# Performance work log

Hardware: AMD Instinct MI355X
Metric: run time of the kernel (lower is better)

Reference implementation:

```python
import jax, jax.numpy as jnp
import numpy as np

D_MODEL = 1024
N_HEADS = 16
D_FF = 4 * D_MODEL
EPS = 1e-5


def _layer_norm(x, g, b):
    mu = jnp.mean(x, axis=-1, keepdims=True)
    var = jnp.mean(jnp.square(x - mu), axis=-1, keepdims=True)
    return (x - mu) * jax.lax.rsqrt(var + EPS) * g + b


def _mha(x, Wq, Wk, Wv, Wo, causal):
    B, S, D = x.shape
    H = N_HEADS
    Dh = D // H
    q = (x @ Wq).reshape(B, S, H, Dh)
    k = (x @ Wk).reshape(B, S, H, Dh)
    v = (x @ Wv).reshape(B, S, H, Dh)
    scores = jnp.einsum('bqhd,bkhd->bhqk', q, k) / jnp.sqrt(jnp.asarray(Dh, x.dtype))
    if causal:
        mask = jnp.tril(jnp.ones((S, S), dtype=bool))  # [S,S] causal mask
        scores = jnp.where(mask, scores, jnp.asarray(-1e9, x.dtype))
    attn = jax.nn.softmax(scores, axis=-1)
    out = jnp.einsum('bhqk,bkhd->bqhd', attn, v).reshape(B, S, D)
    return out @ Wo


def _ffn(x, W1, b1, W2, b2):
    return jax.nn.relu(x @ W1 + b1) @ W2 + b2


def setup_inputs() -> dict:
    key = jax.random.key(0)
    ks = jax.random.split(key, 12)
    sd = 1.0 / np.sqrt(D_MODEL)
    sf = 1.0 / np.sqrt(D_FF)
    B, S = 4, 1024
    return {
        'X': jax.random.normal(ks[0], (B, S, D_MODEL), jnp.float32),
        'Wq1': jax.random.normal(ks[1], (D_MODEL, D_MODEL), jnp.float32) * sd,
        'Wk1': jax.random.normal(ks[2], (D_MODEL, D_MODEL), jnp.float32) * sd,
        'Wv1': jax.random.normal(ks[3], (D_MODEL, D_MODEL), jnp.float32) * sd,
        'Wo1': jax.random.normal(ks[4], (D_MODEL, D_MODEL), jnp.float32) * sd,
        'Wq2': jax.random.normal(ks[5], (D_MODEL, D_MODEL), jnp.float32) * sd,
        'Wk2': jax.random.normal(ks[6], (D_MODEL, D_MODEL), jnp.float32) * sd,
        'Wv2': jax.random.normal(ks[7], (D_MODEL, D_MODEL), jnp.float32) * sd,
        'Wo2': jax.random.normal(ks[8], (D_MODEL, D_MODEL), jnp.float32) * sd,
        'ln_g': jnp.ones((D_MODEL,), jnp.float32),
        'ln_b': jnp.zeros((D_MODEL,), jnp.float32),
        'W1': jax.random.normal(ks[9], (D_MODEL, D_FF), jnp.float32) * sd,
        'b1': jnp.zeros((D_FF,), jnp.float32),
        'W2': jax.random.normal(ks[10], (D_FF, D_MODEL), jnp.float32) * sf,
        'b2': jnp.zeros((D_MODEL,), jnp.float32),
    }


def reference(X, Wq1, Wk1, Wv1, Wo1, Wq2, Wk2, Wv2, Wo2, ln_g, ln_b, W1, b1, W2, b2):
    # Faithful to the torch module (including its unusual residual wiring
    # and the single shared LayerNorm used at all three sites).
    masked = _mha(X, Wq1, Wk1, Wv1, Wo1, causal=True)
    norm_masked = X + _layer_norm(masked, ln_g, ln_b)
    attn2 = _mha(norm_masked, Wq2, Wk2, Wv2, Wo2, causal=False)
    norm_attn2 = attn2 + _layer_norm(attn2, ln_g, ln_b)
    ff = _ffn(norm_attn2, W1, b1, W2, b2)
    return norm_attn2 + _layer_norm(ff, ln_g, ln_b)
```

## Files before the change

### kernel.cpp

```cpp
#include <hip/hip_runtime.h>
#include <hip/hip_bf16.h>

#define D_MODEL 1024
#define N_HEADS 16
#define DH 64
#define D_FF   4096
#define SEQ    1024
#define BATCH  4
#define TOK    (BATCH*SEQ)
#define EPS    1e-5f
#define SCALE  0.125f
#define QSCL   0.18033688f

typedef unsigned short USHORT;
typedef __attribute__((ext_vector_type(8))) short short8v;
typedef __attribute__((ext_vector_type(4))) float f32x4;

__device__ __forceinline__ USHORT f2bf(float f) {
    unsigned int u; __builtin_memcpy(&u, &f, 4);
    u += 0x7fffu + ((u >> 16) & 1u);
    return (USHORT)(u >> 16);
}
__device__ __forceinline__ float bf2f(USHORT s) {
    unsigned int u = ((unsigned int)s) << 16;
    float f; __builtin_memcpy(&f, &u, 4);
    return f;
}

__device__ __forceinline__ short8v ld_frag(const USHORT* lds, int row, int c8) {
    return *reinterpret_cast<const short8v*>(
        &lds[row * 64 + (((c8) ^ (row & 7)) << 3)]);
}
__device__ __forceinline__ short8v ld128(const USHORT* lds, int row, int cu) {
    return *reinterpret_cast<const short8v*>(
        &lds[row * 128 + (((cu) ^ (row & 15)) << 3)]);
}

#define GLDS(gsrc, ldst) \
    __builtin_amdgcn_global_load_lds( \
        (const __attribute__((address_space(1))) void*)(gsrc), \
        (__attribute__((address_space(3))) void*)(ldst), 16, 0, 0)

#define WAITVM(n) asm volatile("s_waitcnt vmcnt(" #n ")" ::: "memory")

__global__ __launch_bounds__(512) void gemm_k256_kernel(
    const USHORT* __restrict__ A, const USHORT* __restrict__ Bt,
    float* __restrict__ Cf, USHORT* __restrict__ Cb, USHORT* __restrict__ Ck,
    USHORT* __restrict__ VtOut,
    int M, int N, int K, const float* __restrict__ bias, int relu, int qkv)
{
    __shared__ USHORT As[2][256 * 64];
    __shared__ USHORT Bs[2][256 * 64];

    const int tid = threadIdx.x;
    const int l   = tid & 63;
    const int w   = tid >> 6;
    const int wr  = w >> 2, wc = w & 3;
    const int lr  = l & 15, lg = l >> 4;

    const int gx  = gridDim.x;
    const int nwg = gx * gridDim.y;
    const int lin = blockIdx.y * gx + blockIdx.x;
    const int swz = (lin & 7) * (nwg >> 3) + (lin >> 3);
    const int m0  = (swz / gx) * 256, n0 = (swz % gx) * 256;

    const USHORT* aS[4]; const USHORT* bS[4]; int dOf[4];
#pragma unroll
    for (int p = 0; p < 4; ++p) {
        const int q = p * 512 + tid;
        const int row = q >> 3, cu = q & 7;
        const int cs = ((cu ^ (row & 7)) << 3);
        aS[p] = A  + (size_t)(m0 + row) * K + cs;
        bS[p] = Bt + (size_t)(n0 + row) * K + cs;
        dOf[p] = (p * 512 + w * 64) * 8;
    }

    auto stage = [&](int buf, int k0) {
#pragma unroll
        for (int p = 0; p < 4; ++p) {
            GLDS(aS[p] + k0, &As[buf][dOf[p]]);
            GLDS(bS[p] + k0, &Bs[buf][dOf[p]]);
        }
    };

    f32x4 acc[8][4];
#pragma unroll
    for (int i = 0; i < 8; ++i)
#pragma unroll
        for (int j = 0; j < 4; ++j) acc[i][j] = (f32x4){0.f, 0.f, 0.f, 0.f};

    const int nk = K >> 6;
    stage(0, 0);

    for (int t = 0; t < nk; ++t) {
        const int cur = t & 1;
        if (t + 1 < nk) {
            stage(cur ^ 1, (t + 1) << 6);
            WAITVM(8);
        } else {
            WAITVM(0);
        }
        __builtin_amdgcn_s_barrier();

#pragma unroll
        for (int ks = 0; ks < 2; ++ks) {
            short8v bfr[4];
#pragma unroll
            for (int ni = 0; ni < 4; ++ni)
                bfr[ni] = ld_frag(Bs[cur], wc * 64 + ni * 16 + lr, ks * 4 + lg);
            __builtin_amdgcn_s_setprio(1);
#pragma unroll
            for (int mi = 0; mi < 8; ++mi) {
                short8v af = ld_frag(As[cur], wr * 128 + mi * 16 + lr, ks * 4 + lg);
#pragma unroll
                for (int ni = 0; ni < 4; ++ni)
                    acc[mi][ni] = __builtin_amdgcn_mfma_f32_16x16x32_bf16(
                        af, bfr[ni], acc[mi][ni], 0, 0, 0);
            }
            __builtin_amdgcn_s_setprio(0);
        }
        __builtin_amdgcn_s_barrier();
    }

    if (qkv) {
#pragma unroll
        for (int mi = 0; mi < 8; ++mi) {
            const int row = m0 + wr * 128 + mi * 16 + (l >> 4) * 4;
#pragma unroll
            for (int ni = 0; ni < 4; ++ni) {
                const int col = n0 + wc * 64 + ni * 16 + lr;
                if (col < 2048) {
                    USHORT* dst = (col < 1024) ? Cb : Ck;
                    const float scl = (col < 1024) ? QSCL : 1.f;
                    const int c = col & 1023;
#pragma unroll
                    for (int j = 0; j < 4; ++j)
                        dst[(size_t)(row + j) * D_MODEL + c] =
                            f2bf(acc[mi][ni][j] * scl);
                } else {
                    const int c = col - 2048;
                    const int bb = row >> 10, jr = row & 1023;
                    const int hh = c >> 6, dd = c & 63;
                    ushort4 pk = make_ushort4(
                        f2bf(acc[mi][ni][0]), f2bf(acc[mi][ni][1]),
                        f2bf(acc[mi][ni][2]), f2bf(acc[mi][ni][3]));
                    *reinterpret_cast<ushort4*>(
                        &VtOut[((size_t)(bb * 16 + hh) * 64 + dd) * 1024 + jr]) = pk;
                }
            }
        }
    } else {
#pragma unroll
        for (int mi = 0; mi < 8; ++mi) {
            const int row = m0 + wr * 128 + mi * 16 + (l >> 4) * 4;
#pragma unroll
            for (int ni = 0; ni < 4; ++ni) {
                const int col = n0 + wc * 64 + ni * 16 + lr;
                const float bv = bias ? bias[col] : 0.f;
#pragma unroll
                for (int j = 0; j < 4; ++j) {
                    float v = acc[mi][ni][j] + bv;
                    if (relu) v = fmaxf(v, 0.f);
                    const size_t idx = (size_t)(row + j) * N + col;
                    if (Cf) Cf[idx] = v;
                    if (Cb) Cb[idx] = f2bf(v);
                }
            }
        }
    }
}

__global__ __launch_bounds__(256) void gemm_k64b_kernel(
    const USHORT* __restrict__ A, const USHORT* __restrict__ Bt,
    float* __restrict__ Cf, USHORT* __restrict__ Cb,
    int M, int N, int K, const float* __restrict__ bias, int relu)
{
    __shared__ USHORT As[3][64 * 64];
    __shared__ USHORT Bs[3][128 * 64];

    const int tid = threadIdx.x;
    const int l   = tid & 63;
    const int w   = tid >> 6;
    const int wr  = w >> 1, wc = w & 1;
    const int lr  = l & 15, lg = l >> 4;

    const int gx  = gridDim.x;
    const int nwg = gx * gridDim.y;
    const int lin = blockIdx.y * gx + blockIdx.x;
    const int swz = (lin & 7) * (nwg >> 3) + (lin >> 3);
    const int m0  = (swz / gx) * 64, n0 = (swz % gx) * 128;

    const int ar0 = tid >> 3,         ac0 = ((tid & 7) ^ (ar0 & 7)) << 3;
    const int ar1 = (256 + tid) >> 3, ac1 = (((256 + tid) & 7) ^ (ar1 & 7)) << 3;
    const USHORT* aS0 = A + (size_t)(m0 + ar0) * K + ac0;
    const USHORT* aS1 = A + (size_t)(m0 + ar1) * K + ac1;
    const int adOf0 = (w * 64) * 8;
    const int adOf1 = (256 + w * 64) * 8;

    const USHORT* bS[4]; int bdOf[4];
#pragma unroll
    for (int p = 0; p < 4; ++p) {
        const int q = p * 256 + tid;
        const int row = q >> 3, cu = q & 7;
        bS[p] = Bt + (size_t)(n0 + row) * K + ((cu ^ (row & 7)) << 3);
        bdOf[p] = (p * 256 + w * 64) * 8;
    }

    auto stage = [&](int buf, int k0) {
        GLDS(aS0 + k0, &As[buf][adOf0]);
        GLDS(aS1 + k0, &As[buf][adOf1]);
#pragma unroll
        for (int p = 0; p < 4; ++p)
            GLDS(bS[p] + k0, &Bs[buf][bdOf[p]]);
    };

    f32x4 acc[2][4];
#pragma unroll
    for (int i = 0; i < 2; ++i)
#pragma unroll
        for (int j = 0; j < 4; ++j) acc[i][j] = (f32x4){0.f, 0.f, 0.f, 0.f};

    const int nk = K >> 6;
    stage(0, 0);
    if (nk > 1) stage(1, 64);

    for (int t = 0; t < nk; ++t) {
        const int cur = t % 3;
        if (t + 1 < nk) { WAITVM(6); } else { WAITVM(0); }
        __builtin_amdgcn_s_barrier();
        if (t + 2 < nk) stage((t + 2) % 3, (t + 2) << 6);

#pragma unroll
        for (int ks = 0; ks < 2; ++ks) {
            short8v af[2], bfr[4];
#pragma unroll
            for (int mi = 0; mi < 2; ++mi)
                af[mi] = ld_frag(As[cur], wr * 32 + mi * 16 + lr, ks * 4 + lg);
#pragma unroll
            for (int ni = 0; ni < 4; ++ni)
                bfr[ni] = ld_frag(Bs[cur], wc * 64 + ni * 16 + lr, ks * 4 + lg);
            __builtin_amdgcn_s_setprio(1);
#pragma unroll
            for (int mi = 0; mi < 2; ++mi)
#pragma unroll
                for (int ni = 0; ni < 4; ++ni)
                    acc[mi][ni] = __builtin_amdgcn_mfma_f32_16x16x32_bf16(
                        af[mi], bfr[ni], acc[mi][ni], 0, 0, 0);
            __builtin_amdgcn_s_setprio(0);
        }
    }

#pragma unroll
    for (int mi = 0; mi < 2; ++mi) {
        const int row = m0 + wr * 32 + mi * 16 + (l >> 4) * 4;
#pragma unroll
        for (int ni = 0; ni < 4; ++ni) {
            const int col = n0 + wc * 64 + ni * 16 + lr;
            const float bv = bias ? bias[col] : 0.f;
#pragma unroll
            for (int j = 0; j < 4; ++j) {
                float v = acc[mi][ni][j] + bv;
                if (relu) v = fmaxf(v, 0.f);
                const size_t idx = (size_t)(row + j) * N + col;
                if (Cf) Cf[idx] = v;
                if (Cb) Cb[idx] = f2bf(v);
            }
        }
    }
}

struct TcvtB4 {
    const float* s0; const float* s1; const float* s2; const float* s3;
    USHORT* d0; USHORT* d1; USHORT* d2; USHORT* d3;
};

__device__ __forceinline__ void tcvt_body(
    const float* __restrict__ W, USHORT* __restrict__ Wt, int K, int N)
{
    __shared__ USHORT L[64][65];
    const int tid = threadIdx.x;
    const int tx = tid & 15, ty = tid >> 4;
    const int n0 = blockIdx.x * 64, k0 = blockIdx.y * 64;
#pragma unroll
    for (int r = 0; r < 4; ++r) {
        int kr = ty + 16 * r;
        float4 v = *reinterpret_cast<const float4*>(
            &W[(size_t)(k0 + kr) * N + n0 + tx * 4]);
        L[tx * 4 + 0][kr] = f2bf(v.x);
        L[tx * 4 + 1][kr] = f2bf(v.y);
        L[tx * 4 + 2][kr] = f2bf(v.z);
        L[tx * 4 + 3][kr] = f2bf(v.w);
    }
    __syncthreads();
#pragma unroll
    for (int r = 0; r < 4; ++r) {
        int nr = ty + 16 * r;
        ushort4 o = make_ushort4(L[nr][tx * 4 + 0], L[nr][tx * 4 + 1],
                                 L[nr][tx * 4 + 2], L[nr][tx * 4 + 3]);
        *reinterpret_cast<ushort4*>(&Wt[(size_t)(n0 + nr) * K + k0 + tx * 4]) = o;
    }
}

__global__ __launch_bounds__(256) void tcvt_kernel(
    const float* __restrict__ W, USHORT* __restrict__ Wt, int K, int N)
{
    tcvt_body(W, Wt, K, N);
}

__global__ __launch_bounds__(256) void tcvt4_kernel(TcvtB4 p, int K, int N)
{
    const int z = blockIdx.z;
    const float* W = (z == 0) ? p.s0 : (z == 1) ? p.s1 : (z == 2) ? p.s2 : p.s3;
    USHORT*    Wt = (z == 0) ? p.d0 : (z == 1) ? p.d1 : (z == 2) ? p.d2 : p.d3;
    tcvt_body(W, Wt, K, N);
}

__global__ __launch_bounds__(256) void f2b_kernel(
    const float* __restrict__ in, USHORT* __restrict__ out, int n4)
{
    int i = blockIdx.x * 256 + threadIdx.x;
    if (i < n4) {
        float4 v = reinterpret_cast<const float4*>(in)[i];
        reinterpret_cast<ushort4*>(out)[i] =
            make_ushort4(f2bf(v.x), f2bf(v.y), f2bf(v.z), f2bf(v.w));
    }
}

__global__ __launch_bounds__(256) void attn_mfma_kernel(
    const USHORT* __restrict__ Q, const USHORT* __restrict__ K,
    const USHORT* __restrict__ Vt, USHORT* __restrict__ O, int causal)
{
    __shared__ USHORT smem[40960];

    const int tid = threadIdx.x;
    const int l  = tid & 63;
    const int w  = tid >> 6;
    const int lr = l & 15;
    const int lg = l >> 4;

    const int lin = blockIdx.y * 16 + blockIdx.x;
    const int swz = (lin & 7) * 128 + (lin >> 3);
    const int qt = swz & 15;
    const int bh = swz >> 4;
    const int h = bh & 15, b = bh >> 4;
    const int q0 = qt * 64;

    const USHORT* gq  = Q  + (size_t)(b * SEQ + q0) * D_MODEL + h * DH;
    const USHORT* gk0 = K  + (size_t)b * SEQ * D_MODEL + h * DH;
    const USHORT* gv0 = Vt + (size_t)bh * DH * SEQ;

    auto stageK = [&](int buf, int kt) {
        USHORT* dst = smem + buf * 8192;
        const size_t base = (size_t)kt * 128 * 1024;
#pragma unroll
        for (int p = 0; p < 4; ++p) {
            const int q = p * 256 + tid;
            const int row = q >> 3, cu = q & 7;
            GLDS(gk0 + base + (size_t)row * 1024 + ((cu ^ (row & 7)) << 3),
                 dst + (p * 256 + w * 64) * 8);
        }
    };
    auto stageV = [&](int buf, int kt) {
        USHORT* dst = smem + 16384 + buf * 8192;
        const int j0 = kt * 128;
#pragma unroll
        for (int p = 0; p < 4; ++p) {
            const int q = p * 256 + tid;
            const int row = q >> 4, cu = q & 15;
            GLDS(gv0 + (size_t)row * 1024 + j0 + ((cu ^ (row & 15)) << 3),
                 dst + (p * 256 + w * 64) * 8);
        }
    };

#pragma unroll
    for (int p = 0; p < 2; ++p) {
        const int q = p * 256 + tid;
        const int row = q >> 3, cu = q & 7;
        GLDS(gq + (size_t)row * 1024 + ((cu ^ (row & 7)) << 3),
             smem + 32768 + (p * 256 + w * 64) * 8);
    }
    stageK(0, 0);
    stageV(0, 0);

    f32x4 oacc[4];
    float m_[4], l_[4];
#pragma unroll
    for (int r = 0; r < 4; ++r) { m_[r] = -1e30f; l_[r] = 0.f; }
#pragma unroll
    for (int d = 0; d < 4; ++d) oacc[d] = (f32x4){0.f, 0.f, 0.f, 0.f};

    __syncthreads();
    short8v qa0 = ld_frag(smem + 32768, w * 16 + lr, lg);
    short8v qa1 = ld_frag(smem + 32768, w * 16 + lr, 4 + lg);
    __syncthreads();
    USHORT* PsW = smem + 32768 + w * 2048;

    const int ntile = causal ? (qt >> 1) + 1 : (SEQ / 128);
    for (int kt = 0; kt < ntile; ++kt) {
        const int cur = kt & 1;
        if (kt + 1 < ntile) {
            stageK(cur ^ 1, kt + 1);
            stageV(cur ^ 1, kt + 1);
        }
        const int j0 = kt * 128;
        const USHORT* KsC = smem + cur * 8192;
        const USHORT* VsC = smem + 16384 + cur * 8192;

        f32x4 sa[8];
        __builtin_amdgcn_s_setprio(1);
#pragma unroll
        for (int jb = 0; jb < 8; ++jb) {
            sa[jb] = (f32x4){0.f, 0.f, 0.f, 0.f};
            sa[jb] = __builtin_amdgcn_mfma_f32_16x16x32_bf16(
                qa0, ld_frag(KsC, jb * 16 + lr, lg), sa[jb], 0, 0, 0);
            sa[jb] = __builtin_amdgcn_mfma_f32_16x16x32_bf16(
                qa1, ld_frag(KsC, jb * 16 + lr, 4 + lg), sa[jb], 0, 0, 0);
        }
        __builtin_amdgcn_s_setprio(0);

        if (causal && kt == ntile - 1) {
#pragma unroll
            for (int jb = 0; jb < 8; ++jb)
#pragma unroll
                for (int r = 0; r < 4; ++r)
                    if ((j0 + jb * 16 + lr) > (q0 + w * 16 + lg * 4 + r))
                        sa[jb][r] = -1e30f;
        }

        float tmloc[4];
#pragma unroll
        for (int r = 0; r < 4; ++r)
            tmloc[r] = fmaxf(fmaxf(fmaxf(sa[0][r], sa[1][r]),
                                   fmaxf(sa[2][r], sa[3][r])),
                             fmaxf(fmaxf(sa[4][r], sa[5][r]),
                                   fmaxf(sa[6][r], sa[7][r])));

        const bool anyf = (tmloc[0] > m_[0] + 8.f) | (tmloc[1] > m_[1] + 8.f) |
                          (tmloc[2] > m_[2] + 8.f) | (tmloc[3] > m_[3] + 8.f);
        const unsigned long long bal = __ballot(anyf);
        if ((bal >> (lg * 16)) & 0xFFFFull) {
#pragma unroll
            for (int r = 0; r < 4; ++r) {
                float tm = tmloc[r];
                tm = fmaxf(tm, __shfl_xor(tm, 1));
                tm = fmaxf(tm, __shfl_xor(tm, 2));
                tm = fmaxf(tm, __shfl_xor(tm, 4));
                tm = fmaxf(tm, __shfl_xor(tm, 8));
                if (tm > m_[r] + 8.f) {
                    float sc = exp2f(m_[r] - tm);
                    l_[r] *= sc;
#pragma unroll
                    for (int d = 0; d < 4; ++d) oacc[d][r] *= sc;
                    m_[r] = tm;
                }
            }
        }

#pragma unroll
        for (int r = 0; r < 4; ++r) {
            float rs_ = 0.f;
#pragma unroll
            for (int jb = 0; jb < 8; ++jb) {
                float p = exp2f(sa[jb][r] - m_[r]);
                sa[jb][r] = p;
                rs_ += p;
            }
            l_[r] += rs_;
        }

#pragma unroll
        for (int jb = 0; jb < 8; ++jb) {
            const int cu = jb * 2 + (lr >> 3), cl = lr & 7;
#pragma unroll
            for (int r = 0; r < 4; ++r) {
                const int row = lg * 4 + r;
                PsW[row * 128 + ((cu ^ (row & 15)) << 3) + cl] = f2bf(sa[jb][r]);
            }
        }

        __builtin_amdgcn_s_setprio(1);
#pragma unroll
        for (int ks = 0; ks < 4; ++ks) {
            short8v pa = ld128(PsW, lr, ks * 4 + lg);
#pragma unroll
            for (int d = 0; d < 4; ++d)
                oacc[d] = __builtin_amdgcn_mfma_f32_16x16x32_bf16(
                    pa, ld128(VsC, d * 16 + lr, ks * 4 + lg), oacc[d], 0, 0, 0);
        }
        __builtin_amdgcn_s_setprio(0);
        __syncthreads();
    }

    USHORT* go = O + (size_t)(b * SEQ + q0 + w * 16) * D_MODEL + h * DH;
#pragma unroll
    for (int r = 0; r < 4; ++r) {
        float lv = l_[r];
        lv += __shfl_xor(lv, 1);
        lv += __shfl_xor(lv, 2);
        lv += __shfl_xor(lv, 4);
        lv += __shfl_xor(lv, 8);
        const float inv = 1.f / lv;
        const int qrow = lg * 4 + r;
#pragma unroll
        for (int d = 0; d < 4; ++d)
            go[(size_t)qrow * D_MODEL + d * 16 + lr] = f2bf(oacc[d][r] * inv);
    }
}

__global__ __launch_bounds__(256) void ln_res_kernel(
    const USHORT* __restrict__ xb, const float* __restrict__ resf,
    const USHORT* __restrict__ resb,
    const float* __restrict__ g, const float* __restrict__ bta,
    float* __restrict__ outf, USHORT* __restrict__ outb)
{
    __shared__ float red[256];
    __shared__ float s_mu, s_rstd;

    const int row = blockIdx.x;
    const int tid = threadIdx.x;
    ushort4 xv = reinterpret_cast<const ushort4*>(xb + (size_t)row * D_MODEL)[tid];
    float vx = bf2f(xv.x), vy = bf2f(xv.y), vz = bf2f(xv.z), vw = bf2f(xv.w);

    red[tid] = vx + vy + vz + vw;
    __syncthreads();
    for (int s = 128; s > 0; s >>= 1) {
        if (tid < s) red[tid] += red[tid + s];
        __syncthreads();
    }
    if (tid == 0) s_mu = red[0] * (1.f / D_MODEL);
    __syncthreads();
    const float mu = s_mu;

    float dx = vx - mu, dy = vy - mu, dz = vz - mu, dw = vw - mu;
    red[tid] = dx * dx + dy * dy + dz * dz + dw * dw;
    __syncthreads();
    for (int s = 128; s > 0; s >>= 1) {
        if (tid < s) red[tid] += red[tid + s];
        __syncthreads();
    }
    if (tid == 0) s_rstd = rsqrtf(red[0] * (1.f / D_MODEL) + EPS);
    __syncthreads();
    const float rstd = s_rstd;

    float4 rv;
    if (resf) {
        rv = reinterpret_cast<const float4*>(resf + (size_t)row * D_MODEL)[tid];
    } else {
        ushort4 rb = reinterpret_cast<const ushort4*>(
            resb + (size_t)row * D_MODEL)[tid];
        rv = make_float4(bf2f(rb.x), bf2f(rb.y), bf2f(rb.z), bf2f(rb.w));
    }
    float4 gv = reinterpret_cast<const float4*>(g)[tid];
    float4 bv = reinterpret_cast<const float4*>(bta)[tid];

    float4 o;
    o.x = rv.x + dx * rstd * gv.x + bv.x;
    o.y = rv.y + dy * rstd * gv.y + bv.y;
    o.z = rv.z + dz * rstd * gv.z + bv.z;
    o.w = rv.w + dw * rstd * gv.w + bv.w;
    reinterpret_cast<float4*>(outf + (size_t)row * D_MODEL)[tid] = o;
    if (outb)
        reinterpret_cast<ushort4*>(outb + (size_t)row * D_MODEL)[tid] =
            make_ushort4(f2bf(o.x), f2bf(o.y), f2bf(o.z), f2bf(o.w));
}

extern "C" void kernel_launch(void* const* d_in, const int* in_sizes, int n_in,
                              void* d_out, int out_size, void* d_ws, size_t ws_size,
                              hipStream_t stream)
{
    const float* X    = (const float*)d_in[0];
    const float* Wq1  = (const float*)d_in[1];
    const float* Wk1  = (const float*)d_in[2];
    const float* Wv1  = (const float*)d_in[3];
    const float* Wo1  = (const float*)d_in[4];
    const float* Wq2  = (const float*)d_in[5];
    const float* Wk2  = (const float*)d_in[6];
    const float* Wv2  = (const float*)d_in[7];
    const float* Wo2  = (const float*)d_in[8];
    const float* ln_g = (const float*)d_in[9];
    const float* ln_b = (const float*)d_in[10];
    const float* W1   = (const float*)d_in[11];
    const float* b1   = (const float*)d_in[12];
    const float* W2   = (const float*)d_in[13];
    const float* b2   = (const float*)d_in[14];

    const size_t MI = 1024 * 1024;
    USHORT* ws16 = (USHORT*)d_ws;
    USHORT* Wqkv1t = ws16;
    USHORT* Wo1t   = ws16 + 3 * MI;
    USHORT* Wqkv2t = ws16 + 4 * MI;
    USHORT* Wo2t   = ws16 + 7 * MI;
    USHORT* W2t    = ws16 + 8 * MI;
    USHORT* Xb     = ws16 + 12 * MI;
    USHORT* W1t    = Xb;
    USHORT* qb     = ws16 + 16 * MI;
    USHORT* kb     = ws16 + 20 * MI;
    USHORT* Vtb    = ws16 + 24 * MI;
    USHORT* t0b    = ws16 + 28 * MI;
    USHORT* hb     = qb;
    USHORT* t2b    = ws16 + 32 * MI;
    USHORT* t1b    = ws16 + 36 * MI;
    float*  t2     = (float*)(ws16 + 40 * MI);

    auto gemm256 = [&](const USHORT* A, const USHORT* Bt, float* Cf, USHORT* Cb,
                       int M, int N, int K, const float* bias, int relu) {
        gemm_k256_kernel<<<dim3(N / 256, M / 256), 512, 0, stream>>>(
            A, Bt, Cf, Cb, nullptr, nullptr, M, N, K, bias, relu, 0);
    };
    auto gemm_qkv = [&](const USHORT* A, const USHORT* Bt) {
        gemm_k256_kernel<<<dim3(3072 / 256, TOK / 256), 512, 0, stream>>>(
            A, Bt, nullptr, qb, kb, Vtb, TOK, 3072, D_MODEL, nullptr, 0, 1);
    };
    auto gemm64b = [&](const USHORT* A, const USHORT* Bt, float* Cf, USHORT* Cb,
                       int M, int N, int K, const float* bias, int relu) {
        gemm_k64b_kernel<<<dim3(N / 128, M / 64), 256, 0, stream>>>(
            A, Bt, Cf, Cb, M, N, K, bias, relu);
    };

    dim3 agrid(SEQ / 64, BATCH * N_HEADS);

    {
        TcvtB4 p1{Wq1, Wk1, Wv1, Wo1,
                  Wqkv1t, Wqkv1t + 1 * MI, Wqkv1t + 2 * MI, Wo1t};
        tcvt4_kernel<<<dim3(16, 16, 4), 256, 0, stream>>>(p1, D_MODEL, D_MODEL);
        TcvtB4 p2{Wq2, Wk2, Wv2, Wo2,
                  Wqkv2t, Wqkv2t + 1 * MI, Wqkv2t + 2 * MI, Wo2t};
        tcvt4_kernel<<<dim3(16, 16, 4), 256, 0, stream>>>(p2, D_MODEL, D_MODEL);
    }
    tcvt_kernel<<<dim3(D_MODEL / 64, D_FF / 64), 256, 0, stream>>>(
        W2, W2t, D_FF, D_MODEL);
    f2b_kernel<<<dim3(4096), 256, 0, stream>>>(X, Xb, TOK * D_MODEL / 4);

    gemm_qkv(Xb, Wqkv1t);
    attn_mfma_kernel<<<agrid, 256, 0, stream>>>(qb, kb, Vtb, t0b, 1);
    gemm64b(t0b, Wo1t, nullptr, t1b, TOK, D_MODEL, D_MODEL, nullptr, 0);
    ln_res_kernel<<<dim3(TOK), 256, 0, stream>>>(t1b, X, nullptr,
                                                 ln_g, ln_b, t2, t2b);
    tcvt_kernel<<<dim3(D_FF / 64, D_MODEL / 64), 256, 0, stream>>>(
        W1, W1t, D_MODEL, D_FF);

    gemm_qkv(t2b, Wqkv2t);
    attn_mfma_kernel<<<agrid, 256, 0, stream>>>(qb, kb, Vtb, t0b, 0);
    gemm64b(t0b, Wo2t, nullptr, t1b, TOK, D_MODEL, D_MODEL, nullptr, 0);
    ln_res_kernel<<<dim3(TOK), 256, 0, stream>>>(t1b, nullptr, t1b,
                                                 ln_g, ln_b, t2, t2b);

    gemm256(t2b, W1t, nullptr, hb, TOK, D_FF, D_MODEL, b1, 1);
    gemm64b(hb, W2t, nullptr, t1b, TOK, D_MODEL, D_FF, b2, 0);
    ln_res_kernel<<<dim3(TOK), 256, 0, stream>>>(t1b, t2, nullptr,
                                                 ln_g, ln_b, (float*)d_out, nullptr);
}
```

Measured before the change: 371.2 us.

## Split-K the narrow-N GEMMs in two and reduce partials in the LayerNorm kernel

The 64x128-tile GEMM used for the output projections and FFN down-projection is replaced by a split-K variant that launches twice as many workgroups, each covering half of K and writing bf16 partials to separate buffers. The LayerNorm/residual kernel now sums the two partials and adds the bias, so the reduction and bias are folded into an existing pass. The pipeline drops from triple to double buffering with an extra barrier per iteration. This adds partial-buffer write/read traffic and bf16 rounding of partials in exchange for better occupancy on the 4096x1024 outputs.

```diff
diff --git a/kernel.cpp b/kernel.cpp
--- a/kernel.cpp
+++ b/kernel.cpp
@@ -170,13 +170,13 @@
     }
 }
 
-__global__ __launch_bounds__(256) void gemm_k64b_kernel(
+__global__ __launch_bounds__(256) void gemm_k64c_kernel(
     const USHORT* __restrict__ A, const USHORT* __restrict__ Bt,
-    float* __restrict__ Cf, USHORT* __restrict__ Cb,
-    int M, int N, int K, const float* __restrict__ bias, int relu)
-{
-    __shared__ USHORT As[3][64 * 64];
-    __shared__ USHORT Bs[3][128 * 64];
+    USHORT* __restrict__ Pa, USHORT* __restrict__ Pb,
+    int M, int N, int K)
+{
+    __shared__ USHORT As[2][64 * 64];
+    __shared__ USHORT Bs[2][128 * 64];
 
     const int tid = threadIdx.x;
     const int l   = tid & 63;
@@ -188,7 +188,13 @@
     const int nwg = gx * gridDim.y;
     const int lin = blockIdx.y * gx + blockIdx.x;
     const int swz = (lin & 7) * (nwg >> 3) + (lin >> 3);
-    const int m0  = (swz / gx) * 64, n0 = (swz % gx) * 128;
+    const int my  = swz / gx;
+    const int mt  = M >> 6;
+    const int part = my / mt;
+    const int m0  = (my % mt) * 64;
+    const int n0  = (swz % gx) * 128;
+    const int koff = part * (K >> 1);
+    USHORT* dst = part ? Pb : Pa;
 
     const int ar0 = tid >> 3,         ac0 = ((tid & 7) ^ (ar0 & 7)) << 3;
     const int ar1 = (256 + tid) >> 3, ac1 = (((256 + tid) & 7) ^ (ar1 & 7)) << 3;
@@ -220,15 +226,18 @@
 #pragma unroll
         for (int j = 0; j < 4; ++j) acc[i][j] = (f32x4){0.f, 0.f, 0.f, 0.f};
 
-    const int nk = K >> 6;
-    stage(0, 0);
-    if (nk > 1) stage(1, 64);
+    const int nk = K >> 7;
+    stage(0, koff);
 
     for (int t = 0; t < nk; ++t) {
-        const int cur = t % 3;
-        if (t + 1 < nk) { WAITVM(6); } else { WAITVM(0); }
+        const int cur = t & 1;
+        if (t + 1 < nk) {
+            stage(cur ^ 1, koff + ((t + 1) << 6));
+            WAITVM(6);
+        } else {
+            WAITVM(0);
+        }
         __builtin_amdgcn_s_barrier();
-        if (t + 2 < nk) stage((t + 2) % 3, (t + 2) << 6);
 
 #pragma unroll
         for (int ks = 0; ks < 2; ++ks) {
@@ -248,6 +257,7 @@
                         af[mi], bfr[ni], acc[mi][ni], 0, 0, 0);
             __builtin_amdgcn_s_setprio(0);
         }
+        __builtin_amdgcn_s_barrier();
     }
 
 #pragma unroll
@@ -256,15 +266,9 @@
 #pragma unroll
         for (int ni = 0; ni < 4; ++ni) {
             const int col = n0 + wc * 64 + ni * 16 + lr;
-            const float bv = bias ? bias[col] : 0.f;
-#pragma unroll
-            for (int j = 0; j < 4; ++j) {
-                float v = acc[mi][ni][j] + bv;
-                if (relu) v = fmaxf(v, 0.f);
-                const size_t idx = (size_t)(row + j) * N + col;
-                if (Cf) Cf[idx] = v;
-                if (Cb) Cb[idx] = f2bf(v);
-            }
+#pragma unroll
+            for (int j = 0; j < 4; ++j)
+                dst[(size_t)(row + j) * N + col] = f2bf(acc[mi][ni][j]);
         }
     }
 }
@@ -508,8 +512,9 @@
 }
 
 __global__ __launch_bounds__(256) void ln_res_kernel(
-    const USHORT* __restrict__ xb, const float* __restrict__ resf,
-    const USHORT* __restrict__ resb,
+    const USHORT* __restrict__ xb, const USHORT* __restrict__ xb2,
+    const float* __restrict__ biasx,
+    const float* __restrict__ resf, const USHORT* __restrict__ resb,
     const float* __restrict__ g, const float* __restrict__ bta,
     float* __restrict__ outf, USHORT* __restrict__ outb)
 {
@@ -520,6 +525,15 @@
     const int tid = threadIdx.x;
     ushort4 xv = reinterpret_cast<const ushort4*>(xb + (size_t)row * D_MODEL)[tid];
     float vx = bf2f(xv.x), vy = bf2f(xv.y), vz = bf2f(xv.z), vw = bf2f(xv.w);
+    if (xb2) {
+        ushort4 x2 = reinterpret_cast<const ushort4*>(
+            xb2 + (size_t)row * D_MODEL)[tid];
+        vx += bf2f(x2.x); vy += bf2f(x2.y); vz += bf2f(x2.z); vw += bf2f(x2.w);
+    }
+    if (biasx) {
+        float4 bx = reinterpret_cast<const float4*>(biasx)[tid];
+        vx += bx.x; vy += bx.y; vz += bx.z; vw += bx.w;
+    }
 
     red[tid] = vx + vy + vz + vw;
     __syncthreads();
@@ -545,10 +559,12 @@
     float4 rv;
     if (resf) {
         rv = reinterpret_cast<const float4*>(resf + (size_t)row * D_MODEL)[tid];
-    } else {
+    } else if (resb) {
         ushort4 rb = reinterpret_cast<const ushort4*>(
             resb + (size_t)row * D_MODEL)[tid];
         rv = make_float4(bf2f(rb.x), bf2f(rb.y), bf2f(rb.z), bf2f(rb.w));
+    } else {
+        rv = make_float4(vx, vy, vz, vw);
     }
     float4 gv = reinterpret_cast<const float4*>(g)[tid];
     float4 bv = reinterpret_cast<const float4*>(bta)[tid];
@@ -587,6 +603,7 @@
     const size_t MI = 1024 * 1024;
     USHORT* ws16 = (USHORT*)d_ws;
     USHORT* Wqkv1t = ws16;
+    USHORT* scr0   = ws16;
     USHORT* Wo1t   = ws16 + 3 * MI;
     USHORT* Wqkv2t = ws16 + 4 * MI;
     USHORT* Wo2t   = ws16 + 7 * MI;
@@ -611,10 +628,10 @@
         gemm_k256_kernel<<<dim3(3072 / 256, TOK / 256), 512, 0, stream>>>(
             A, Bt, nullptr, qb, kb, Vtb, TOK, 3072, D_MODEL, nullptr, 0, 1);
     };
-    auto gemm64b = [&](const USHORT* A, const USHORT* Bt, float* Cf, USHORT* Cb,
-                       int M, int N, int K, const float* bias, int relu) {
-        gemm_k64b_kernel<<<dim3(N / 128, M / 64), 256, 0, stream>>>(
-            A, Bt, Cf, Cb, M, N, K, bias, relu);
+    auto gemm64c = [&](const USHORT* A, const USHORT* Bt, USHORT* Pa, USHORT* Pb,
+                       int M, int N, int K) {
+        gemm_k64c_kernel<<<dim3(N / 128, (M / 64) * 2), 256, 0, stream>>>(
+            A, Bt, Pa, Pb, M, N, K);
     };
 
     dim3 agrid(SEQ / 64, BATCH * N_HEADS);
@@ -633,20 +650,21 @@
 
     gemm_qkv(Xb, Wqkv1t);
     attn_mfma_kernel<<<agrid, 256, 0, stream>>>(qb, kb, Vtb, t0b, 1);
-    gemm64b(t0b, Wo1t, nullptr, t1b, TOK, D_MODEL, D_MODEL, nullptr, 0);
-    ln_res_kernel<<<dim3(TOK), 256, 0, stream>>>(t1b, X, nullptr,
+    gemm64c(t0b, Wo1t, t2b, t1b, TOK, D_MODEL, D_MODEL);
+    ln_res_kernel<<<dim3(TOK), 256, 0, stream>>>(t2b, t1b, nullptr, X, nullptr,
                                                  ln_g, ln_b, t2, t2b);
     tcvt_kernel<<<dim3(D_FF / 64, D_MODEL / 64), 256, 0, stream>>>(
         W1, W1t, D_MODEL, D_FF);
 
     gemm_qkv(t2b, Wqkv2t);
     attn_mfma_kernel<<<agrid, 256, 0, stream>>>(qb, kb, Vtb, t0b, 0);
-    gemm64b(t0b, Wo2t, nullptr, t1b, TOK, D_MODEL, D_MODEL, nullptr, 0);
-    ln_res_kernel<<<dim3(TOK), 256, 0, stream>>>(t1b, nullptr, t1b,
+    gemm64c(t0b, Wo2t, scr0, t1b, TOK, D_MODEL, D_MODEL);
+    ln_res_kernel<<<dim3(TOK), 256, 0, stream>>>(scr0, t1b, nullptr,
+                                                 nullptr, nullptr,
                                                  ln_g, ln_b, t2, t2b);
 
     gemm256(t2b, W1t, nullptr, hb, TOK, D_FF, D_MODEL, b1, 1);
-    gemm64b(hb, W2t, nullptr, t1b, TOK, D_MODEL, D_FF, b2, 0);
-    ln_res_kernel<<<dim3(TOK), 256, 0, stream>>>(t1b, t2, nullptr,
+    gemm64c(hb, W2t, t2b, t1b, TOK, D_MODEL, D_FF);
+    ln_res_kernel<<<dim3(TOK), 256, 0, stream>>>(t2b, t1b, b2, t2, nullptr,
                                                  ln_g, ln_b, (float*)d_out, nullptr);
 }
```

Result: no change. 371.7 us (+0.1%).
